# Kernel optimization log

Hardware: AMD Instinct MI355X
Metric: run time of the kernel (lower is better)

Reference implementation:

```python
import jax, jax.numpy as jnp
import numpy as np

# Module hyperparameters (init_kwargs)
H, W, C = 80, 80, 6
N = H * W
THETA_ALPHA = 8.0   # bilateral spatial bandwidth
THETA_BETA = 0.15   # bilateral color bandwidth (feature_map in [0,1))
THETA_GAMMA = 3.0   # spatial-only bandwidth
NUM_ITER = 5


def setup_inputs() -> dict:
    key = jax.random.key(0)
    k1, k2, k3, k4, k5, k6 = jax.random.split(key, 6)
    eye = jnp.eye(C, dtype=jnp.float32)
    return {
        'unary_potentials': jax.random.normal(k1, (1, H, W, C), jnp.float32),
        'feature_map': jax.random.uniform(k2, (H, W, 3), jnp.float32),
        # Potts init (-I) / identity inits, perturbed so grads are nontrivial
        'compatibility_matrix': -eye + 0.05 * jax.random.normal(k3, (C, C), jnp.float32),
        'local_global_potential': eye + 0.05 * jax.random.normal(k4, (C, C), jnp.float32),
        'spatial_ker_weights': eye + 0.05 * jax.random.normal(k5, (C, C), jnp.float32),
        'bilateral_ker_weights': eye + 0.05 * jax.random.normal(k6, (C, C), jnp.float32),
    }


def _sqdist(a):
    # a: [N, d] -> pairwise squared distances [N, N]
    s = jnp.sum(a * a, axis=-1)
    return s[:, None] + s[None, :] - 2.0 * (a @ a.T)


def _kernels(feature_map):
    # Exact dense Gaussian kernels (the math the permutohedral filter approximates)
    yy, xx = jnp.meshgrid(jnp.arange(H, dtype=jnp.float32),
                          jnp.arange(W, dtype=jnp.float32), indexing='ij')
    pos = jnp.stack([yy.ravel(), xx.ravel()], axis=-1)       # [N, 2]
    d2p = _sqdist(pos)                                       # [N, N]
    feat = feature_map.reshape(N, 3)
    d2f = _sqdist(feat)                                      # [N, N]
    Ks = jnp.exp(-d2p / (2.0 * THETA_GAMMA ** 2))            # spatial kernel
    Kb = jnp.exp(-d2p / (2.0 * THETA_ALPHA ** 2) - d2f / (2.0 * THETA_BETA ** 2))
    return Ks, Kb


def _forward(unary_potentials, feature_map, compatibility_matrix,
             local_global_potential, spatial_ker_weights, bilateral_ker_weights):
    Ks, Kb = _kernels(feature_map)
    norm_s = jnp.sum(Ks, axis=1)  # = high_dim_filter(ones), per-pixel normalizer [N]
    norm_b = jnp.sum(Kb, axis=1)
    unary = jnp.transpose(unary_potentials[0], (2, 0, 1)).reshape(C, N)  # [C, N]

    def message(sm):  # sm: [C, N]
        sp = spatial_ker_weights @ ((sm @ Ks) / norm_s)   # kernels symmetric
        bl = bilateral_ker_weights @ ((sm @ Kb) / norm_b)
        return sp + bl

    def elbo_for_label(lg_col):  # lg_col = local_global_potential[:, y], shape [C]
        q = unary
        sm = jax.nn.softmax(q, axis=0)
        for _ in range(NUM_ITER):
            sm = jax.nn.softmax(q, axis=0)
            pairwise = compatibility_matrix @ message(sm)
            # einsum('ij,jkl->ikl', W, onehot_y) == W[:, y] broadcast over pixels
            q = unary + lg_col[:, None] - pairwise
        # ELBO uses sm from the last iteration (softmax of the pre-update q)
        unary_term = jnp.sum(sm * unary)
        lg_term = jnp.dot(lg_col, jnp.sum(sm, axis=1))
        pairwise_term = -jnp.sum(message(sm) * sm)
        entropy = -jnp.sum(sm * jnp.log(sm + 1e-10))
        return unary_term + lg_term + entropy + pairwise_term

    lg_cols = local_global_potential.T  # row y is column y of W
    return jax.vmap(elbo_for_label)(lg_cols)  # [C] elbos, one per label y


def reference(unary_potentials, feature_map, compatibility_matrix,
              local_global_potential, spatial_ker_weights, bilateral_ker_weights):
    return _forward(unary_potentials, feature_map, compatibility_matrix,
                    local_global_potential, spatial_ker_weights, bilateral_ker_weights)
```

## Files before the change

### kernel.cpp

```cpp
#include <hip/hip_runtime.h>
#include <hip/hip_bf16.h>
#include <math.h>

#define HH 80
#define WW 80
#define NPIX 6400
#define CC 36
#define CCP 48
#define NC 6
#define NUM_ITER 5
#define JS 20
#define SLICE (NPIX / JS)
#define JTILES (SLICE / 32)
#define IBLK 50

typedef __attribute__((ext_vector_type(8))) short bfrag;
typedef __attribute__((ext_vector_type(4))) float f32x4;
typedef __attribute__((ext_vector_type(2))) float f32x2;

__device__ __constant__ const float kSA = 0.08838834764831845f;
__device__ __constant__ const float kSB = 5.663898078577187f;
__device__ __constant__ const float kRS = 7.11111111f;

__device__ inline unsigned short f2bf(float f) {
    unsigned u = __builtin_bit_cast(unsigned, f);
    unsigned r = (u + 0x7FFFu + ((u >> 16) & 1u)) >> 16;
    return (unsigned short)r;
}

__global__ __launch_bounds__(256) void k_init(const float* __restrict__ unary,
                                              const float* __restrict__ feat,
                                              float* __restrict__ sm,
                                              unsigned short* __restrict__ smbT,
                                              float* __restrict__ pf,
                                              float* __restrict__ out) {
    int i = blockIdx.x * 256 + threadIdx.x;
    if (blockIdx.x == 0 && threadIdx.x < NC) out[threadIdx.x] = 0.f;
    if (i >= NPIX) return;
    int y = i / WW, x = i - y * WW;
    pf[0 * NPIX + i] = kSA * (float)y;
    pf[1 * NPIX + i] = kSA * (float)x;
    pf[2 * NPIX + i] = kSB * feat[i * 3 + 0];
    pf[3 * NPIX + i] = kSB * feat[i * 3 + 1];
    pf[4 * NPIX + i] = kSB * feat[i * 3 + 2];
    float v[NC], mx = -1e30f;
#pragma unroll
    for (int c = 0; c < NC; c++) { v[c] = unary[i * NC + c]; mx = fmaxf(mx, v[c]); }
    float sum = 0.f;
#pragma unroll
    for (int c = 0; c < NC; c++) { v[c] = __expf(v[c] - mx); sum += v[c]; }
    float inv = 1.f / sum;
#pragma unroll
    for (int l = 0; l < NC; l++) {
#pragma unroll
        for (int c = 0; c < NC; c++) {
            float s = v[c] * inv;
            sm[(size_t)i * CC + l * NC + c] = s;
            smbT[(size_t)(l * 8 + c) * NPIX + i] = f2bf(s);
        }
        smbT[(size_t)(l * 8 + 6) * NPIX + i] = 0x3F80;
        smbT[(size_t)(l * 8 + 7) * NPIX + i] = 0;
    }
}

__global__ __launch_bounds__(256) void k_bil(const unsigned short* __restrict__ smbT,
                                             const float* __restrict__ pf,
                                             unsigned* __restrict__ part) {
    int tid = threadIdx.x, bid = blockIdx.x;
    int s = bid / IBLK, ib = bid - s * IBLK;
    int j00 = s * SLICE;
    int wv = tid >> 6, lane = tid & 63, r = lane & 15, gq = lane >> 4;
    int it0 = (ib * 4 + wv) * 32;
    int iA = it0 + r, iB = iA + 16;

    const float* py = pf;
    const float* px = pf + NPIX;
    const float* p0 = pf + 2 * NPIX;
    const float* p1 = pf + 3 * NPIX;
    const float* p2 = pf + 4 * NPIX;

    float yA = py[iA], xA = px[iA], fA0 = p0[iA], fA1 = p1[iA], fA2 = p2[iA];
    float yB = py[iB], xB = px[iB], fB0 = p0[iB], fB1 = p1[iB], fB2 = p2[iB];
    const f32x2 rs2 = {kRS, kRS};

    f32x4 abA[3], asA[3], abB[3], asB[3];
#pragma unroll
    for (int t = 0; t < 3; t++) {
        abA[t] = (f32x4){0.f, 0.f, 0.f, 0.f};
        asA[t] = (f32x4){0.f, 0.f, 0.f, 0.f};
        abB[t] = (f32x4){0.f, 0.f, 0.f, 0.f};
        asB[t] = (f32x4){0.f, 0.f, 0.f, 0.f};
    }

    for (int jt = 0; jt < JTILES; jt++) {
        int jb = j00 + jt * 32 + 8 * gq;
        f32x4 yj0 = *(const f32x4*)(py + jb), yj1 = *(const f32x4*)(py + jb + 4);
        f32x4 xj0 = *(const f32x4*)(px + jb), xj1 = *(const f32x4*)(px + jb + 4);
        f32x4 c00 = *(const f32x4*)(p0 + jb), c01 = *(const f32x4*)(p0 + jb + 4);
        f32x4 c10 = *(const f32x4*)(p1 + jb), c11 = *(const f32x4*)(p1 + jb + 4);
        f32x4 c20 = *(const f32x4*)(p2 + jb), c21 = *(const f32x4*)(p2 + jb + 4);
        bfrag Bf[3];
#pragma unroll
        for (int t = 0; t < 3; t++)
            Bf[t] = *(const bfrag*)(smbT + (size_t)(16 * t + r) * NPIX + jb);

        union { unsigned u[4]; bfrag v; } Ab, As, Bb, Bs;
#pragma unroll
        for (int p = 0; p < 4; p++) {
            f32x4 ysrc = (p < 2) ? yj0 : yj1;
            f32x4 xsrc = (p < 2) ? xj0 : xj1;
            f32x4 s0 = (p < 2) ? c00 : c01;
            f32x4 s1 = (p < 2) ? c10 : c11;
            f32x4 s2 = (p < 2) ? c20 : c21;
            int e = (p & 1) * 2;
            f32x2 yj = {ysrc[e], ysrc[e + 1]};
            f32x2 xj = {xsrc[e], xsrc[e + 1]};
            f32x2 u0 = {s0[e], s0[e + 1]};
            f32x2 u1 = {s1[e], s1[e + 1]};
            f32x2 u2 = {s2[e], s2[e + 1]};

            f32x2 dy = (f32x2){yA, yA} - yj;
            f32x2 dx = (f32x2){xA, xA} - xj;
            f32x2 sp = dy * dy; sp = dx * dx + sp;
            f32x2 d0 = (f32x2){fA0, fA0} - u0;
            f32x2 d1 = (f32x2){fA1, fA1} - u1;
            f32x2 d2 = (f32x2){fA2, fA2} - u2;
            f32x2 a = d0 * d0 + sp; a = d1 * d1 + a; a = d2 * d2 + a;
            f32x2 aspt = rs2 * sp;
            float wb0 = __builtin_amdgcn_exp2f(-a[0]);
            float wb1 = __builtin_amdgcn_exp2f(-a[1]);
            float ws0 = __builtin_amdgcn_exp2f(-aspt[0]);
            float ws1 = __builtin_amdgcn_exp2f(-aspt[1]);
            asm("v_cvt_pk_bf16_f32 %0, %1, %2" : "=v"(Ab.u[p]) : "v"(wb0), "v"(wb1));
            asm("v_cvt_pk_bf16_f32 %0, %1, %2" : "=v"(As.u[p]) : "v"(ws0), "v"(ws1));

            dy = (f32x2){yB, yB} - yj;
            dx = (f32x2){xB, xB} - xj;
            sp = dy * dy; sp = dx * dx + sp;
            d0 = (f32x2){fB0, fB0} - u0;
            d1 = (f32x2){fB1, fB1} - u1;
            d2 = (f32x2){fB2, fB2} - u2;
            a = d0 * d0 + sp; a = d1 * d1 + a; a = d2 * d2 + a;
            aspt = rs2 * sp;
            wb0 = __builtin_amdgcn_exp2f(-a[0]);
            wb1 = __builtin_amdgcn_exp2f(-a[1]);
            ws0 = __builtin_amdgcn_exp2f(-aspt[0]);
            ws1 = __builtin_amdgcn_exp2f(-aspt[1]);
            asm("v_cvt_pk_bf16_f32 %0, %1, %2" : "=v"(Bb.u[p]) : "v"(wb0), "v"(wb1));
            asm("v_cvt_pk_bf16_f32 %0, %1, %2" : "=v"(Bs.u[p]) : "v"(ws0), "v"(ws1));
        }
#pragma unroll
        for (int t = 0; t < 3; t++) {
            abA[t] = __builtin_amdgcn_mfma_f32_16x16x32_bf16(Ab.v, Bf[t], abA[t], 0, 0, 0);
            asA[t] = __builtin_amdgcn_mfma_f32_16x16x32_bf16(As.v, Bf[t], asA[t], 0, 0, 0);
            abB[t] = __builtin_amdgcn_mfma_f32_16x16x32_bf16(Bb.v, Bf[t], abB[t], 0, 0, 0);
            asB[t] = __builtin_amdgcn_mfma_f32_16x16x32_bf16(Bs.v, Bf[t], asB[t], 0, 0, 0);
        }
    }
#pragma unroll
    for (int t = 0; t < 3; t++)
#pragma unroll
        for (int d = 0; d < 4; d++) {
            int irow = it0 + 4 * gq + d;
            unsigned pkA, pkB;
            asm("v_cvt_pk_bf16_f32 %0, %1, %2" : "=v"(pkA) : "v"(abA[t][d]), "v"(asA[t][d]));
            asm("v_cvt_pk_bf16_f32 %0, %1, %2" : "=v"(pkB) : "v"(abB[t][d]), "v"(asB[t][d]));
            part[((size_t)s * NPIX + irow) * CCP + 16 * t + r] = pkA;
            part[((size_t)s * NPIX + irow + 16) * CCP + 16 * t + r] = pkB;
        }
}

template <bool LAST>
__global__ __launch_bounds__(256) void k_update(const unsigned* __restrict__ part,
                                                const float* __restrict__ unary,
                                                const float* __restrict__ SW,
                                                const float* __restrict__ BW,
                                                const float* __restrict__ CM,
                                                const float* __restrict__ LG,
                                                float* __restrict__ sm,
                                                unsigned short* __restrict__ smbT,
                                                float* __restrict__ out) {
    __shared__ float sSW[36], sBW[36], sCM[36], sLG[36];
    __shared__ float bins[NC];
    int tid = threadIdx.x;
    if (tid < 36) { sSW[tid] = SW[tid]; sBW[tid] = BW[tid]; sCM[tid] = CM[tid]; sLG[tid] = LG[tid]; }
    if (LAST && tid < NC) bins[tid] = 0.f;
    __syncthreads();
    int t = blockIdx.x * 256 + tid;
    int n = t / NC, l = t - n * NC;

    float fb[NC], fs[NC], nb = 0.f, ns = 0.f;
#pragma unroll
    for (int c = 0; c < NC; c++) { fb[c] = 0.f; fs[c] = 0.f; }
    for (int s = 0; s < JS; s++) {
        const uint4* pp = (const uint4*)(part + ((size_t)s * NPIX + n) * CCP + l * 8);
        uint4 v0 = pp[0], v1 = pp[1];
        unsigned d[7] = {v0.x, v0.y, v0.z, v0.w, v1.x, v1.y, v1.z};
#pragma unroll
        for (int c = 0; c < NC; c++) {
            fb[c] += __builtin_bit_cast(float, d[c] << 16);
            fs[c] += __builtin_bit_cast(float, d[c] & 0xFFFF0000u);
        }
        nb += __builtin_bit_cast(float, d[6] << 16);
        ns += __builtin_bit_cast(float, d[6] & 0xFFFF0000u);
    }
    float invb = 1.f / nb, invs = 1.f / ns;
#pragma unroll
    for (int c = 0; c < NC; c++) { fb[c] *= invb; fs[c] *= invs; }

    float m[NC];
#pragma unroll
    for (int c = 0; c < NC; c++) {
        float a = 0.f;
#pragma unroll
        for (int cp = 0; cp < NC; cp++)
            a += sSW[c * NC + cp] * fs[cp] + sBW[c * NC + cp] * fb[cp];
        m[c] = a;
    }
    const float* up = unary + (size_t)n * NC;
    if (!LAST) {
        float qv[NC], mxq = -1e30f;
#pragma unroll
        for (int c = 0; c < NC; c++) {
            float pw = 0.f;
#pragma unroll
            for (int cp = 0; cp < NC; cp++) pw += sCM[c * NC + cp] * m[cp];
            qv[c] = up[c] + sLG[c * NC + l] - pw;
            mxq = fmaxf(mxq, qv[c]);
        }
        float e[NC], ssum = 0.f;
#pragma unroll
        for (int c = 0; c < NC; c++) { e[c] = __expf(qv[c] - mxq); ssum += e[c]; }
        float inv = 1.f / ssum;
        float* sp = sm + (size_t)n * CC + l * NC;
#pragma unroll
        for (int c = 0; c < NC; c++) {
            float sv = e[c] * inv;
            sp[c] = sv;
            smbT[(size_t)(l * 8 + c) * NPIX + n] = f2bf(sv);
        }
    } else {
        const float* sp = sm + (size_t)n * CC + l * NC;
        float v = 0.f;
#pragma unroll
        for (int c = 0; c < NC; c++) {
            float sv = sp[c];
            v += sv * (up[c] + sLG[c * NC + l] - logf(sv + 1e-10f) - m[c]);
        }
        atomicAdd(&bins[l], v);
        __syncthreads();
        if (tid < NC) atomicAdd(&out[tid], bins[tid]);
    }
}

extern "C" void kernel_launch(void* const* d_in, const int* in_sizes, int n_in,
                              void* d_out, int out_size, void* d_ws, size_t ws_size,
                              hipStream_t stream) {
    const float* unary = (const float*)d_in[0];
    const float* feat  = (const float*)d_in[1];
    const float* CM    = (const float*)d_in[2];
    const float* LG    = (const float*)d_in[3];
    const float* SW    = (const float*)d_in[4];
    const float* BW    = (const float*)d_in[5];
    float* out = (float*)d_out;

    float* ws = (float*)d_ws;
    float* pf = ws;
    float* sm = pf + (size_t)5 * NPIX;
    unsigned short* smbT = (unsigned short*)(sm + (size_t)CC * NPIX);
    unsigned* part = (unsigned*)(ws + (size_t)65 * NPIX);

    k_init<<<25, 256, 0, stream>>>(unary, feat, sm, smbT, pf, out);

    for (int it = 0; it < NUM_ITER; it++) {
        k_bil<<<IBLK * JS, 256, 0, stream>>>(smbT, pf, part);
        if (it < NUM_ITER - 1)
            k_update<false><<<150, 256, 0, stream>>>(part, unary, SW, BW, CM, LG,
                                                     sm, smbT, out);
        else
            k_update<true><<<150, 256, 0, stream>>>(part, unary, SW, BW, CM, LG,
                                                    sm, smbT, out);
    }
}
```

Baseline: 278.4 us.

## Stage bilateral j-slice in LDS and shard update reduction across lanes

k_bil now cooperatively loads the block's j-slice of position/feature data and the transposed bf16 softmax rows into shared memory, using an XOR swizzle for the bf16 tile, then reads tiles from LDS instead of global memory. k_update splits the 20-slice partial-sum reduction across 4 lanes and combines them with xor shuffles, launching four times as many blocks so the reduction has more parallelism. This trades LDS capacity (about 37 KB per block, which may lower occupancy) and a block-wide barrier for fewer redundant global loads across the four waves.

```diff
diff --git a/kernel.cpp b/kernel.cpp
--- a/kernel.cpp
+++ b/kernel.cpp
@@ -13,6 +13,7 @@
 #define SLICE (NPIX / JS)
 #define JTILES (SLICE / 32)
 #define IBLK 50
+#define SHARD 4
 
 typedef __attribute__((ext_vector_type(8))) short bfrag;
 typedef __attribute__((ext_vector_type(4))) float f32x4;
@@ -66,21 +67,32 @@
 __global__ __launch_bounds__(256) void k_bil(const unsigned short* __restrict__ smbT,
                                              const float* __restrict__ pf,
                                              unsigned* __restrict__ part) {
+    __shared__ __align__(16) float s_pf[5 * SLICE];
+    __shared__ __align__(16) unsigned short s_smT[48 * SLICE];
     int tid = threadIdx.x, bid = blockIdx.x;
     int s = bid / IBLK, ib = bid - s * IBLK;
     int j00 = s * SLICE;
+
+    for (int idx = tid; idx < 5 * SLICE; idx += 256) {
+        int a = idx / SLICE, jl = idx - a * SLICE;
+        s_pf[idx] = pf[(size_t)a * NPIX + j00 + jl];
+    }
+    for (int slot = tid; slot < 48 * (SLICE / 8); slot += 256) {
+        int row = slot / (SLICE / 8), c16 = slot - row * (SLICE / 8);
+        uint4 v = *(const uint4*)(smbT + (size_t)row * NPIX + j00 + c16 * 8);
+        unsigned off = (unsigned)(row * (SLICE * 2) + c16 * 16) ^ ((unsigned)(row & 7) << 4);
+        *(uint4*)((char*)s_smT + off) = v;
+    }
+    __syncthreads();
+
     int wv = tid >> 6, lane = tid & 63, r = lane & 15, gq = lane >> 4;
     int it0 = (ib * 4 + wv) * 32;
     int iA = it0 + r, iB = iA + 16;
 
-    const float* py = pf;
-    const float* px = pf + NPIX;
-    const float* p0 = pf + 2 * NPIX;
-    const float* p1 = pf + 3 * NPIX;
-    const float* p2 = pf + 4 * NPIX;
-
-    float yA = py[iA], xA = px[iA], fA0 = p0[iA], fA1 = p1[iA], fA2 = p2[iA];
-    float yB = py[iB], xB = px[iB], fB0 = p0[iB], fB1 = p1[iB], fB2 = p2[iB];
+    float yA = pf[iA], xA = pf[NPIX + iA];
+    float fA0 = pf[2 * NPIX + iA], fA1 = pf[3 * NPIX + iA], fA2 = pf[4 * NPIX + iA];
+    float yB = pf[iB], xB = pf[NPIX + iB];
+    float fB0 = pf[2 * NPIX + iB], fB1 = pf[3 * NPIX + iB], fB2 = pf[4 * NPIX + iB];
     const f32x2 rs2 = {kRS, kRS};
 
     f32x4 abA[3], asA[3], abB[3], asB[3];
@@ -93,16 +105,25 @@
     }
 
     for (int jt = 0; jt < JTILES; jt++) {
-        int jb = j00 + jt * 32 + 8 * gq;
-        f32x4 yj0 = *(const f32x4*)(py + jb), yj1 = *(const f32x4*)(py + jb + 4);
-        f32x4 xj0 = *(const f32x4*)(px + jb), xj1 = *(const f32x4*)(px + jb + 4);
-        f32x4 c00 = *(const f32x4*)(p0 + jb), c01 = *(const f32x4*)(p0 + jb + 4);
-        f32x4 c10 = *(const f32x4*)(p1 + jb), c11 = *(const f32x4*)(p1 + jb + 4);
-        f32x4 c20 = *(const f32x4*)(p2 + jb), c21 = *(const f32x4*)(p2 + jb + 4);
+        int jl = jt * 32 + 8 * gq;
+        const float* pl = s_pf + jl;
+        f32x4 yj0 = *(const f32x4*)(pl);
+        f32x4 yj1 = *(const f32x4*)(pl + 4);
+        f32x4 xj0 = *(const f32x4*)(pl + SLICE);
+        f32x4 xj1 = *(const f32x4*)(pl + SLICE + 4);
+        f32x4 c00 = *(const f32x4*)(pl + 2 * SLICE);
+        f32x4 c01 = *(const f32x4*)(pl + 2 * SLICE + 4);
+        f32x4 c10 = *(const f32x4*)(pl + 3 * SLICE);
+        f32x4 c11 = *(const f32x4*)(pl + 3 * SLICE + 4);
+        f32x4 c20 = *(const f32x4*)(pl + 4 * SLICE);
+        f32x4 c21 = *(const f32x4*)(pl + 4 * SLICE + 4);
         bfrag Bf[3];
 #pragma unroll
-        for (int t = 0; t < 3; t++)
-            Bf[t] = *(const bfrag*)(smbT + (size_t)(16 * t + r) * NPIX + jb);
+        for (int t = 0; t < 3; t++) {
+            unsigned off = (unsigned)((16 * t + r) * (SLICE * 2) + jl * 2)
+                           ^ ((unsigned)(r & 7) << 4);
+            Bf[t] = *(const bfrag*)((const char*)s_smT + off);
+        }
 
         union { unsigned u[4]; bfrag v; } Ab, As, Bb, Bs;
 #pragma unroll
@@ -186,13 +207,16 @@
     if (tid < 36) { sSW[tid] = SW[tid]; sBW[tid] = BW[tid]; sCM[tid] = CM[tid]; sLG[tid] = LG[tid]; }
     if (LAST && tid < NC) bins[tid] = 0.f;
     __syncthreads();
-    int t = blockIdx.x * 256 + tid;
-    int n = t / NC, l = t - n * NC;
+    int u = blockIdx.x * 256 + tid;
+    int pr = u >> 2, h = u & 3;
+    int n = pr / NC, l = pr - n * NC;
 
     float fb[NC], fs[NC], nb = 0.f, ns = 0.f;
 #pragma unroll
     for (int c = 0; c < NC; c++) { fb[c] = 0.f; fs[c] = 0.f; }
-    for (int s = 0; s < JS; s++) {
+#pragma unroll
+    for (int s5 = 0; s5 < JS / SHARD; s5++) {
+        int s = h * (JS / SHARD) + s5;
         const uint4* pp = (const uint4*)(part + ((size_t)s * NPIX + n) * CCP + l * 8);
         uint4 v0 = pp[0], v1 = pp[1];
         unsigned d[7] = {v0.x, v0.y, v0.z, v0.w, v1.x, v1.y, v1.z};
@@ -204,6 +228,16 @@
         nb += __builtin_bit_cast(float, d[6] << 16);
         ns += __builtin_bit_cast(float, d[6] & 0xFFFF0000u);
     }
+#pragma unroll
+    for (int st = 1; st < SHARD; st <<= 1) {
+#pragma unroll
+        for (int c = 0; c < NC; c++) {
+            fb[c] += __shfl_xor(fb[c], st);
+            fs[c] += __shfl_xor(fs[c], st);
+        }
+        nb += __shfl_xor(nb, st);
+        ns += __shfl_xor(ns, st);
+    }
     float invb = 1.f / nb, invs = 1.f / ns;
 #pragma unroll
     for (int c = 0; c < NC; c++) { fb[c] *= invb; fs[c] *= invs; }
@@ -219,35 +253,39 @@
     }
     const float* up = unary + (size_t)n * NC;
     if (!LAST) {
-        float qv[NC], mxq = -1e30f;
-#pragma unroll
-        for (int c = 0; c < NC; c++) {
-            float pw = 0.f;
-#pragma unroll
-            for (int cp = 0; cp < NC; cp++) pw += sCM[c * NC + cp] * m[cp];
-            qv[c] = up[c] + sLG[c * NC + l] - pw;
-            mxq = fmaxf(mxq, qv[c]);
-        }
-        float e[NC], ssum = 0.f;
-#pragma unroll
-        for (int c = 0; c < NC; c++) { e[c] = __expf(qv[c] - mxq); ssum += e[c]; }
-        float inv = 1.f / ssum;
-        float* sp = sm + (size_t)n * CC + l * NC;
-#pragma unroll
-        for (int c = 0; c < NC; c++) {
-            float sv = e[c] * inv;
-            sp[c] = sv;
-            smbT[(size_t)(l * 8 + c) * NPIX + n] = f2bf(sv);
+        if (h == 0) {
+            float qv[NC], mxq = -1e30f;
+#pragma unroll
+            for (int c = 0; c < NC; c++) {
+                float pw = 0.f;
+#pragma unroll
+                for (int cp = 0; cp < NC; cp++) pw += sCM[c * NC + cp] * m[cp];
+                qv[c] = up[c] + sLG[c * NC + l] - pw;
+                mxq = fmaxf(mxq, qv[c]);
+            }
+            float e[NC], ssum = 0.f;
+#pragma unroll
+            for (int c = 0; c < NC; c++) { e[c] = __expf(qv[c] - mxq); ssum += e[c]; }
+            float inv = 1.f / ssum;
+            float* sp = sm + (size_t)n * CC + l * NC;
+#pragma unroll
+            for (int c = 0; c < NC; c++) {
+                float sv = e[c] * inv;
+                sp[c] = sv;
+                smbT[(size_t)(l * 8 + c) * NPIX + n] = f2bf(sv);
+            }
         }
     } else {
-        const float* sp = sm + (size_t)n * CC + l * NC;
-        float v = 0.f;
-#pragma unroll
-        for (int c = 0; c < NC; c++) {
-            float sv = sp[c];
-            v += sv * (up[c] + sLG[c * NC + l] - logf(sv + 1e-10f) - m[c]);
-        }
-        atomicAdd(&bins[l], v);
+        if (h == 0) {
+            const float* sp = sm + (size_t)n * CC + l * NC;
+            float v = 0.f;
+#pragma unroll
+            for (int c = 0; c < NC; c++) {
+                float sv = sp[c];
+                v += sv * (up[c] + sLG[c * NC + l] - logf(sv + 1e-10f) - m[c]);
+            }
+            atomicAdd(&bins[l], v);
+        }
         __syncthreads();
         if (tid < NC) atomicAdd(&out[tid], bins[tid]);
     }
@@ -275,10 +313,10 @@
     for (int it = 0; it < NUM_ITER; it++) {
         k_bil<<<IBLK * JS, 256, 0, stream>>>(smbT, pf, part);
         if (it < NUM_ITER - 1)
-            k_update<false><<<150, 256, 0, stream>>>(part, unary, SW, BW, CM, LG,
+            k_update<false><<<600, 256, 0, stream>>>(part, unary, SW, BW, CM, LG,
                                                      sm, smbT, out);
         else
-            k_update<true><<<150, 256, 0, stream>>>(part, unary, SW, BW, CM, LG,
+            k_update<true><<<600, 256, 0, stream>>>(part, unary, SW, BW, CM, LG,
                                                     sm, smbT, out);
     }
 }
```

Measured after the change: 284.8 us. 1.02x slower.

## Double-buffer B fragments, stage bil output via LDS, shard update reduction

Applied to the files above, without the earlier changes.

The bilateral kernel now prefetches the next tile's bf16 softmax fragments while the current tile computes its weights, alternating between two register buffers. Its output is staged in shared memory and written back as coalesced 16-byte stores instead of scattered 4-byte writes. The update kernel splits the 20-slice partial reduction across 4 lanes, combines them with xor shuffles, and runs on 4x more blocks to raise memory parallelism. In exchange it uses more registers and LDS, and three of every four update lanes sit idle during the softmax stage.

```diff
diff --git a/kernel.cpp b/kernel.cpp
--- a/kernel.cpp
+++ b/kernel.cpp
@@ -13,6 +13,8 @@
 #define SLICE (NPIX / JS)
 #define JTILES (SLICE / 32)
 #define IBLK 50
+#define SHARD 4
+#define LROW 52
 
 typedef __attribute__((ext_vector_type(8))) short bfrag;
 typedef __attribute__((ext_vector_type(4))) float f32x4;
@@ -66,11 +68,12 @@
 __global__ __launch_bounds__(256) void k_bil(const unsigned short* __restrict__ smbT,
                                              const float* __restrict__ pf,
                                              unsigned* __restrict__ part) {
+    __shared__ unsigned s_out[128 * LROW];
     int tid = threadIdx.x, bid = blockIdx.x;
     int s = bid / IBLK, ib = bid - s * IBLK;
     int j00 = s * SLICE;
     int wv = tid >> 6, lane = tid & 63, r = lane & 15, gq = lane >> 4;
-    int it0 = (ib * 4 + wv) * 32;
+    int it0 = ib * 128 + wv * 32;
     int iA = it0 + r, iB = iA + 16;
 
     const float* py = pf;
@@ -92,82 +95,101 @@
         asB[t] = (f32x4){0.f, 0.f, 0.f, 0.f};
     }
 
-    for (int jt = 0; jt < JTILES; jt++) {
-        int jb = j00 + jt * 32 + 8 * gq;
-        f32x4 yj0 = *(const f32x4*)(py + jb), yj1 = *(const f32x4*)(py + jb + 4);
-        f32x4 xj0 = *(const f32x4*)(px + jb), xj1 = *(const f32x4*)(px + jb + 4);
-        f32x4 c00 = *(const f32x4*)(p0 + jb), c01 = *(const f32x4*)(p0 + jb + 4);
-        f32x4 c10 = *(const f32x4*)(p1 + jb), c11 = *(const f32x4*)(p1 + jb + 4);
-        f32x4 c20 = *(const f32x4*)(p2 + jb), c21 = *(const f32x4*)(p2 + jb + 4);
-        bfrag Bf[3];
-#pragma unroll
-        for (int t = 0; t < 3; t++)
-            Bf[t] = *(const bfrag*)(smbT + (size_t)(16 * t + r) * NPIX + jb);
-
-        union { unsigned u[4]; bfrag v; } Ab, As, Bb, Bs;
-#pragma unroll
-        for (int p = 0; p < 4; p++) {
-            f32x4 ysrc = (p < 2) ? yj0 : yj1;
-            f32x4 xsrc = (p < 2) ? xj0 : xj1;
-            f32x4 s0 = (p < 2) ? c00 : c01;
-            f32x4 s1 = (p < 2) ? c10 : c11;
-            f32x4 s2 = (p < 2) ? c20 : c21;
-            int e = (p & 1) * 2;
-            f32x2 yj = {ysrc[e], ysrc[e + 1]};
-            f32x2 xj = {xsrc[e], xsrc[e + 1]};
-            f32x2 u0 = {s0[e], s0[e + 1]};
-            f32x2 u1 = {s1[e], s1[e + 1]};
-            f32x2 u2 = {s2[e], s2[e + 1]};
-
-            f32x2 dy = (f32x2){yA, yA} - yj;
-            f32x2 dx = (f32x2){xA, xA} - xj;
-            f32x2 sp = dy * dy; sp = dx * dx + sp;
-            f32x2 d0 = (f32x2){fA0, fA0} - u0;
-            f32x2 d1 = (f32x2){fA1, fA1} - u1;
-            f32x2 d2 = (f32x2){fA2, fA2} - u2;
-            f32x2 a = d0 * d0 + sp; a = d1 * d1 + a; a = d2 * d2 + a;
-            f32x2 aspt = rs2 * sp;
-            float wb0 = __builtin_amdgcn_exp2f(-a[0]);
-            float wb1 = __builtin_amdgcn_exp2f(-a[1]);
-            float ws0 = __builtin_amdgcn_exp2f(-aspt[0]);
-            float ws1 = __builtin_amdgcn_exp2f(-aspt[1]);
-            asm("v_cvt_pk_bf16_f32 %0, %1, %2" : "=v"(Ab.u[p]) : "v"(wb0), "v"(wb1));
-            asm("v_cvt_pk_bf16_f32 %0, %1, %2" : "=v"(As.u[p]) : "v"(ws0), "v"(ws1));
-
-            dy = (f32x2){yB, yB} - yj;
-            dx = (f32x2){xB, xB} - xj;
-            sp = dy * dy; sp = dx * dx + sp;
-            d0 = (f32x2){fB0, fB0} - u0;
-            d1 = (f32x2){fB1, fB1} - u1;
-            d2 = (f32x2){fB2, fB2} - u2;
-            a = d0 * d0 + sp; a = d1 * d1 + a; a = d2 * d2 + a;
-            aspt = rs2 * sp;
-            wb0 = __builtin_amdgcn_exp2f(-a[0]);
-            wb1 = __builtin_amdgcn_exp2f(-a[1]);
-            ws0 = __builtin_amdgcn_exp2f(-aspt[0]);
-            ws1 = __builtin_amdgcn_exp2f(-aspt[1]);
-            asm("v_cvt_pk_bf16_f32 %0, %1, %2" : "=v"(Bb.u[p]) : "v"(wb0), "v"(wb1));
-            asm("v_cvt_pk_bf16_f32 %0, %1, %2" : "=v"(Bs.u[p]) : "v"(ws0), "v"(ws1));
-        }
-#pragma unroll
-        for (int t = 0; t < 3; t++) {
-            abA[t] = __builtin_amdgcn_mfma_f32_16x16x32_bf16(Ab.v, Bf[t], abA[t], 0, 0, 0);
-            asA[t] = __builtin_amdgcn_mfma_f32_16x16x32_bf16(As.v, Bf[t], asA[t], 0, 0, 0);
-            abB[t] = __builtin_amdgcn_mfma_f32_16x16x32_bf16(Bb.v, Bf[t], abB[t], 0, 0, 0);
-            asB[t] = __builtin_amdgcn_mfma_f32_16x16x32_bf16(Bs.v, Bf[t], asB[t], 0, 0, 0);
-        }
-    }
+#define LOADB(BF, JT) do {                                                      \
+        int _jb = j00 + (JT) * 32 + 8 * gq;                                     \
+        BF[0] = *(const bfrag*)(smbT + (size_t)(r) * NPIX + _jb);               \
+        BF[1] = *(const bfrag*)(smbT + (size_t)(16 + r) * NPIX + _jb);          \
+        BF[2] = *(const bfrag*)(smbT + (size_t)(32 + r) * NPIX + _jb);          \
+    } while (0)
+
+#define COMPUTE(JT, BF) do {                                                    \
+        int jb = j00 + (JT) * 32 + 8 * gq;                                      \
+        f32x4 yj0 = *(const f32x4*)(py + jb), yj1 = *(const f32x4*)(py + jb + 4);\
+        f32x4 xj0 = *(const f32x4*)(px + jb), xj1 = *(const f32x4*)(px + jb + 4);\
+        f32x4 c00 = *(const f32x4*)(p0 + jb), c01 = *(const f32x4*)(p0 + jb + 4);\
+        f32x4 c10 = *(const f32x4*)(p1 + jb), c11 = *(const f32x4*)(p1 + jb + 4);\
+        f32x4 c20 = *(const f32x4*)(p2 + jb), c21 = *(const f32x4*)(p2 + jb + 4);\
+        union { unsigned u[4]; bfrag v; } Ab, As, Bb, Bs;                       \
+        _Pragma("unroll")                                                       \
+        for (int p = 0; p < 4; p++) {                                           \
+            f32x4 ysrc = (p < 2) ? yj0 : yj1;                                   \
+            f32x4 xsrc = (p < 2) ? xj0 : xj1;                                   \
+            f32x4 s0 = (p < 2) ? c00 : c01;                                     \
+            f32x4 s1 = (p < 2) ? c10 : c11;                                     \
+            f32x4 s2 = (p < 2) ? c20 : c21;                                     \
+            int e = (p & 1) * 2;                                                \
+            f32x2 yj = {ysrc[e], ysrc[e + 1]};                                  \
+            f32x2 xj = {xsrc[e], xsrc[e + 1]};                                  \
+            f32x2 u0 = {s0[e], s0[e + 1]};                                      \
+            f32x2 u1 = {s1[e], s1[e + 1]};                                      \
+            f32x2 u2 = {s2[e], s2[e + 1]};                                      \
+            f32x2 dy = (f32x2){yA, yA} - yj;                                    \
+            f32x2 dx = (f32x2){xA, xA} - xj;                                    \
+            f32x2 sp = dy * dy; sp = dx * dx + sp;                              \
+            f32x2 d0 = (f32x2){fA0, fA0} - u0;                                  \
+            f32x2 d1 = (f32x2){fA1, fA1} - u1;                                  \
+            f32x2 d2 = (f32x2){fA2, fA2} - u2;                                  \
+            f32x2 a = d0 * d0 + sp; a = d1 * d1 + a; a = d2 * d2 + a;           \
+            f32x2 aspt = rs2 * sp;                                              \
+            float wb0 = __builtin_amdgcn_exp2f(-a[0]);                          \
+            float wb1 = __builtin_amdgcn_exp2f(-a[1]);                          \
+            float ws0 = __builtin_amdgcn_exp2f(-aspt[0]);                       \
+            float ws1 = __builtin_amdgcn_exp2f(-aspt[1]);                       \
+            asm("v_cvt_pk_bf16_f32 %0, %1, %2" : "=v"(Ab.u[p]) : "v"(wb0), "v"(wb1)); \
+            asm("v_cvt_pk_bf16_f32 %0, %1, %2" : "=v"(As.u[p]) : "v"(ws0), "v"(ws1)); \
+            dy = (f32x2){yB, yB} - yj;                                          \
+            dx = (f32x2){xB, xB} - xj;                                          \
+            sp = dy * dy; sp = dx * dx + sp;                                    \
+            d0 = (f32x2){fB0, fB0} - u0;                                        \
+            d1 = (f32x2){fB1, fB1} - u1;                                        \
+            d2 = (f32x2){fB2, fB2} - u2;                                        \
+            a = d0 * d0 + sp; a = d1 * d1 + a; a = d2 * d2 + a;                 \
+            aspt = rs2 * sp;                                                    \
+            wb0 = __builtin_amdgcn_exp2f(-a[0]);                                \
+            wb1 = __builtin_amdgcn_exp2f(-a[1]);                                \
+            ws0 = __builtin_amdgcn_exp2f(-aspt[0]);                             \
+            ws1 = __builtin_amdgcn_exp2f(-aspt[1]);                             \
+            asm("v_cvt_pk_bf16_f32 %0, %1, %2" : "=v"(Bb.u[p]) : "v"(wb0), "v"(wb1)); \
+            asm("v_cvt_pk_bf16_f32 %0, %1, %2" : "=v"(Bs.u[p]) : "v"(ws0), "v"(ws1)); \
+        }                                                                       \
+        _Pragma("unroll")                                                       \
+        for (int t = 0; t < 3; t++) {                                           \
+            abA[t] = __builtin_amdgcn_mfma_f32_16x16x32_bf16(Ab.v, BF[t], abA[t], 0, 0, 0); \
+            asA[t] = __builtin_amdgcn_mfma_f32_16x16x32_bf16(As.v, BF[t], asA[t], 0, 0, 0); \
+            abB[t] = __builtin_amdgcn_mfma_f32_16x16x32_bf16(Bb.v, BF[t], abB[t], 0, 0, 0); \
+            asB[t] = __builtin_amdgcn_mfma_f32_16x16x32_bf16(Bs.v, BF[t], asB[t], 0, 0, 0); \
+        }                                                                       \
+    } while (0)
+
+    bfrag Bf0[3], Bf1[3];
+    LOADB(Bf0, 0);
+#pragma unroll
+    for (int jp = 0; jp < JTILES / 2; jp++) {
+        LOADB(Bf1, 2 * jp + 1);
+        COMPUTE(2 * jp, Bf0);
+        if (jp < JTILES / 2 - 1) LOADB(Bf0, 2 * jp + 2);
+        COMPUTE(2 * jp + 1, Bf1);
+    }
+
+    int lrowA = wv * 32 + 4 * gq;
 #pragma unroll
     for (int t = 0; t < 3; t++)
 #pragma unroll
         for (int d = 0; d < 4; d++) {
-            int irow = it0 + 4 * gq + d;
             unsigned pkA, pkB;
             asm("v_cvt_pk_bf16_f32 %0, %1, %2" : "=v"(pkA) : "v"(abA[t][d]), "v"(asA[t][d]));
             asm("v_cvt_pk_bf16_f32 %0, %1, %2" : "=v"(pkB) : "v"(abB[t][d]), "v"(asB[t][d]));
-            part[((size_t)s * NPIX + irow) * CCP + 16 * t + r] = pkA;
-            part[((size_t)s * NPIX + irow + 16) * CCP + 16 * t + r] = pkB;
-        }
+            s_out[(lrowA + d) * LROW + 16 * t + r] = pkA;
+            s_out[(lrowA + d + 16) * LROW + 16 * t + r] = pkB;
+        }
+    __syncthreads();
+    uint4* pout = (uint4*)(part + ((size_t)s * NPIX + ib * 128) * CCP);
+#pragma unroll
+    for (int k = 0; k < 6; k++) {
+        int g4 = tid + k * 256;
+        int row = g4 / 12, c = (g4 - row * 12) * 4;
+        pout[g4] = *(const uint4*)(s_out + row * LROW + c);
+    }
 }
 
 template <bool LAST>
@@ -186,13 +208,16 @@
     if (tid < 36) { sSW[tid] = SW[tid]; sBW[tid] = BW[tid]; sCM[tid] = CM[tid]; sLG[tid] = LG[tid]; }
     if (LAST && tid < NC) bins[tid] = 0.f;
     __syncthreads();
-    int t = blockIdx.x * 256 + tid;
-    int n = t / NC, l = t - n * NC;
+    int u = blockIdx.x * 256 + tid;
+    int pr = u >> 2, h = u & 3;
+    int n = pr / NC, l = pr - n * NC;
 
     float fb[NC], fs[NC], nb = 0.f, ns = 0.f;
 #pragma unroll
     for (int c = 0; c < NC; c++) { fb[c] = 0.f; fs[c] = 0.f; }
-    for (int s = 0; s < JS; s++) {
+#pragma unroll
+    for (int s5 = 0; s5 < JS / SHARD; s5++) {
+        int s = h * (JS / SHARD) + s5;
         const uint4* pp = (const uint4*)(part + ((size_t)s * NPIX + n) * CCP + l * 8);
         uint4 v0 = pp[0], v1 = pp[1];
         unsigned d[7] = {v0.x, v0.y, v0.z, v0.w, v1.x, v1.y, v1.z};
@@ -204,6 +229,16 @@
         nb += __builtin_bit_cast(float, d[6] << 16);
         ns += __builtin_bit_cast(float, d[6] & 0xFFFF0000u);
     }
+#pragma unroll
+    for (int st = 1; st < SHARD; st <<= 1) {
+#pragma unroll
+        for (int c = 0; c < NC; c++) {
+            fb[c] += __shfl_xor(fb[c], st);
+            fs[c] += __shfl_xor(fs[c], st);
+        }
+        nb += __shfl_xor(nb, st);
+        ns += __shfl_xor(ns, st);
+    }
     float invb = 1.f / nb, invs = 1.f / ns;
 #pragma unroll
     for (int c = 0; c < NC; c++) { fb[c] *= invb; fs[c] *= invs; }
@@ -219,35 +254,39 @@
     }
     const float* up = unary + (size_t)n * NC;
     if (!LAST) {
-        float qv[NC], mxq = -1e30f;
-#pragma unroll
-        for (int c = 0; c < NC; c++) {
-            float pw = 0.f;
-#pragma unroll
-            for (int cp = 0; cp < NC; cp++) pw += sCM[c * NC + cp] * m[cp];
-            qv[c] = up[c] + sLG[c * NC + l] - pw;
-            mxq = fmaxf(mxq, qv[c]);
-        }
-        float e[NC], ssum = 0.f;
-#pragma unroll
-        for (int c = 0; c < NC; c++) { e[c] = __expf(qv[c] - mxq); ssum += e[c]; }
-        float inv = 1.f / ssum;
-        float* sp = sm + (size_t)n * CC + l * NC;
-#pragma unroll
-        for (int c = 0; c < NC; c++) {
-            float sv = e[c] * inv;
-            sp[c] = sv;
-            smbT[(size_t)(l * 8 + c) * NPIX + n] = f2bf(sv);
+        if (h == 0) {
+            float qv[NC], mxq = -1e30f;
+#pragma unroll
+            for (int c = 0; c < NC; c++) {
+                float pw = 0.f;
+#pragma unroll
+                for (int cp = 0; cp < NC; cp++) pw += sCM[c * NC + cp] * m[cp];
+                qv[c] = up[c] + sLG[c * NC + l] - pw;
+                mxq = fmaxf(mxq, qv[c]);
+            }
+            float e[NC], ssum = 0.f;
+#pragma unroll
+            for (int c = 0; c < NC; c++) { e[c] = __expf(qv[c] - mxq); ssum += e[c]; }
+            float inv = 1.f / ssum;
+            float* sp = sm + (size_t)n * CC + l * NC;
+#pragma unroll
+            for (int c = 0; c < NC; c++) {
+                float sv = e[c] * inv;
+                sp[c] = sv;
+                smbT[(size_t)(l * 8 + c) * NPIX + n] = f2bf(sv);
+            }
         }
     } else {
-        const float* sp = sm + (size_t)n * CC + l * NC;
-        float v = 0.f;
-#pragma unroll
-        for (int c = 0; c < NC; c++) {
-            float sv = sp[c];
-            v += sv * (up[c] + sLG[c * NC + l] - logf(sv + 1e-10f) - m[c]);
-        }
-        atomicAdd(&bins[l], v);
+        if (h == 0) {
+            const float* sp = sm + (size_t)n * CC + l * NC;
+            float v = 0.f;
+#pragma unroll
+            for (int c = 0; c < NC; c++) {
+                float sv = sp[c];
+                v += sv * (up[c] + sLG[c * NC + l] - logf(sv + 1e-10f) - m[c]);
+            }
+            atomicAdd(&bins[l], v);
+        }
         __syncthreads();
         if (tid < NC) atomicAdd(&out[tid], bins[tid]);
     }
@@ -275,10 +314,10 @@
     for (int it = 0; it < NUM_ITER; it++) {
         k_bil<<<IBLK * JS, 256, 0, stream>>>(smbT, pf, part);
         if (it < NUM_ITER - 1)
-            k_update<false><<<150, 256, 0, stream>>>(part, unary, SW, BW, CM, LG,
+            k_update<false><<<600, 256, 0, stream>>>(part, unary, SW, BW, CM, LG,
                                                      sm, smbT, out);
         else
-            k_update<true><<<150, 256, 0, stream>>>(part, unary, SW, BW, CM, LG,
+            k_update<true><<<600, 256, 0, stream>>>(part, unary, SW, BW, CM, LG,
                                                     sm, smbT, out);
     }
 }
```

After: 303.7 us. +9.1%, slower.
